# Kernel optimization log

Hardware: AMD Instinct MI355X
Metric: run time of the kernel (lower is better)

Reference implementation:

```python
import jax, jax.numpy as jnp
import numpy as np

NUM_CLASSES = 10
GAMMA = 1.0
EPS = 1e-12


def setup_inputs() -> dict:
    key = jax.random.key(0)
    k1, k2, k3, k4 = jax.random.split(key, 4)
    x = jax.random.normal(k1, (1024, 64), dtype=jnp.float32)
    exemplars = jax.random.normal(k2, (50000, 64), dtype=jnp.float32)
    exemplar_labels = jax.random.randint(k3, (50000,), 0, NUM_CLASSES)
    # beta_raw initialized as softplus^{-1}(init_beta) with init_beta=1.0
    init_beta = 1.0
    beta_raw = jnp.array([np.log(np.exp(init_beta) - 1.0)], dtype=jnp.float32)
    return {"x": x, "exemplars": exemplars, "exemplar_labels": exemplar_labels,
            "beta_raw": beta_raw}


def reference(x, exemplars, exemplar_labels, beta_raw):
    # Squared Euclidean distances (weight_diag == ones) via GEMM expansion:
    # d2[b, e] = ||x_b||^2 + ||e_e||^2 - 2 <x_b, e_e>
    x2 = jnp.sum(x * x, axis=-1, keepdims=True)            # (B, 1)
    e2 = jnp.sum(exemplars * exemplars, axis=-1)           # (Ne,)
    d2 = x2 + e2[None, :] - 2.0 * (x @ exemplars.T)        # (B, Ne)
    d2 = jnp.maximum(d2, 0.0)  # true sq-dist is nonneg; guards GEMM round-off
    beta = jax.nn.softplus(beta_raw[0])
    sims = jnp.exp(-beta * d2)                              # (B, Ne)
    # scatter-add similarities into per-class bins: (C, B) -> (B, C)
    class_sims = jax.ops.segment_sum(sims.T, exemplar_labels,
                                     num_segments=NUM_CLASSES).T
    logits = GAMMA * jnp.log(class_sims + EPS)
    return logits
```

## Files before the change

kernel.cpp:

```cpp
#include <hip/hip_runtime.h>


#define NB      1024
#define NE      50000
#define NE_PAD  50176
#define NCHUNK  98
#define KD      64
#define NC      10
#define SROWS   64
#define NSTAGE  8
#define LROW    72

using half8   = __attribute__((ext_vector_type(8))) _Float16;
using half4v  = __attribute__((ext_vector_type(4))) _Float16;
using floatx4 = __attribute__((ext_vector_type(4))) float;

__device__ __forceinline__ float softplus_f(float x) {
  return (x > 20.f) ? x : log1pf(__expf(x));
}

__global__ __launch_bounds__(256) void prep_kernel(
    const float* __restrict__ x, const float* __restrict__ ex,
    const int* __restrict__ labels, const float* __restrict__ beta_raw,
    _Float16* __restrict__ ex_h, float* __restrict__ ce,
    _Float16* __restrict__ x_h, float* __restrict__ cb,
    int* __restrict__ lab_pad)
{
  const int tid = threadIdx.x;
  const float beta = softplus_f(beta_raw[0]);

  const int row = blockIdx.x * 16 + (tid >> 4);
  const int l16 = tid & 15;

  if (row < NE_PAD) {
    float4 v = make_float4(0.f, 0.f, 0.f, 0.f);
    if (row < NE) v = ((const float4*)ex)[row * 16 + l16];
    half4v hv = { (_Float16)v.x, (_Float16)v.y, (_Float16)v.z, (_Float16)v.w };
    *(half4v*)(ex_h + (size_t)row * KD + l16 * 4) = hv;
    float s = v.x*v.x + v.y*v.y + v.z*v.z + v.w*v.w;
    #pragma unroll
    for (int m = 1; m < 16; m <<= 1) s += __shfl_xor(s, m, 64);
    if (l16 == 0) ce[row] = (row < NE) ? (-beta * s) : -1e30f;
    if (l16 == 1) lab_pad[row] = (row < NE) ? labels[row] : 0;
  } else {
    const int rx = row - NE_PAD;
    float4 v = ((const float4*)x)[rx * 16 + l16];
    half4v hv = { (_Float16)v.x, (_Float16)v.y, (_Float16)v.z, (_Float16)v.w };
    *(half4v*)(x_h + (size_t)rx * KD + l16 * 4) = hv;
    float s = v.x*v.x + v.y*v.y + v.z*v.z + v.w*v.w;
    #pragma unroll
    for (int m = 1; m < 16; m <<= 1) s += __shfl_xor(s, m, 64);
    if (l16 == 0) cb[rx] = -beta * s;
  }
}

__global__ __launch_bounds__(256) void main_kernel(
    const _Float16* __restrict__ ex_h, const float* __restrict__ ce,
    const _Float16* __restrict__ x_h, const float* __restrict__ cb,
    const int* __restrict__ lab_pad, const float* __restrict__ beta_raw,
    float* __restrict__ part)
{
  __shared__ _Float16 Ah[2][SROWS * LROW];
  __shared__ float    Ce[2][SROWS];
  __shared__ int      Lb[2][SROWS];

  const int tid  = threadIdx.x;
  const int wave = tid >> 6;
  const int lane = tid & 63;
  const int l15  = lane & 15;
  const int quad = lane >> 4;

  const int btile = blockIdx.x;
  const int chunk = blockIdx.y;
  const int e0    = chunk * 512;
  const int bm    = btile * 64 + wave * 16;

  const float beta = softplus_f(beta_raw[0]);
  const float s2 = 2.f * beta;

  const half8* xrow = (const half8*)(x_h + (size_t)(bm + l15) * KD);
  const half8 bx0 = xrow[quad];
  const half8 bx1 = xrow[quad + 4];
  const float cbl = cb[bm + l15];

  const int srow = tid >> 2;
  const int scol = tid & 3;
  const _Float16* gsrc = ex_h + (size_t)(e0 + srow) * KD + scol * 16;
  const int lofs = srow * LROW + scol * 16;

  half8 pr0 = *(const half8*)(gsrc);
  half8 pr1 = *(const half8*)(gsrc + 8);
  float prc = 0.f; int prl = 0;
  if (wave == 0) prc = ce[e0 + lane];
  if (wave == 1) prl = lab_pad[e0 + lane];

  *(half8*)(&Ah[0][lofs])     = pr0;
  *(half8*)(&Ah[0][lofs + 8]) = pr1;
  if (wave == 0) Ce[0][lane] = prc;
  if (wave == 1) Lb[0][lane] = prl;
  __syncthreads();

  floatx4 acc = {0.f, 0.f, 0.f, 0.f};

  for (int st = 0; st < NSTAGE; ++st) {
    const int b = st & 1;

    if (st + 1 < NSTAGE) {
      const _Float16* g = gsrc + (size_t)(st + 1) * SROWS * KD;
      pr0 = *(const half8*)(g);
      pr1 = *(const half8*)(g + 8);
      if (wave == 0) prc = ce[e0 + (st + 1) * SROWS + lane];
      if (wave == 1) prl = lab_pad[e0 + (st + 1) * SROWS + lane];
    }

    #pragma unroll
    for (int sub = 0; sub < 4; ++sub) {
      const int abase = (sub * 16 + l15) * LROW + quad * 8;
      const half8 ae0 = *(const half8*)(&Ah[b][abase]);
      const half8 ae1 = *(const half8*)(&Ah[b][abase + 32]);
      const float4 ce4 = *(const float4*)(&Ce[b][sub * 16 + quad * 4]);
      const int4   lb4 = *(const int4*)(&Lb[b][sub * 16 + quad * 4]);

      floatx4 d = {0.f, 0.f, 0.f, 0.f};
      d = __builtin_amdgcn_mfma_f32_16x16x32_f16(ae0, bx0, d, 0, 0, 0);
      d = __builtin_amdgcn_mfma_f32_16x16x32_f16(ae1, bx1, d, 0, 0, 0);

      const float cef[4] = { ce4.x, ce4.y, ce4.z, ce4.w };
      half4v p;
      #pragma unroll
      for (int r = 0; r < 4; ++r) {
        const float t = fminf(fmaf(s2, d[r], cbl + cef[r]), 0.f);
        p[r] = (_Float16)__expf(t);
      }

      half4v oh;
      oh[0] = (lb4.x == l15) ? (_Float16)1.f : (_Float16)0.f;
      oh[1] = (lb4.y == l15) ? (_Float16)1.f : (_Float16)0.f;
      oh[2] = (lb4.z == l15) ? (_Float16)1.f : (_Float16)0.f;
      oh[3] = (lb4.w == l15) ? (_Float16)1.f : (_Float16)0.f;

      acc = __builtin_amdgcn_mfma_f32_16x16x16f16(oh, p, acc, 0, 0, 0);
    }

    if (st + 1 < NSTAGE) {
      __syncthreads();
      const int nb = (st + 1) & 1;
      *(half8*)(&Ah[nb][lofs])     = pr0;
      *(half8*)(&Ah[nb][lofs + 8]) = pr1;
      if (wave == 0) Ce[nb][lane] = prc;
      if (wave == 1) Lb[nb][lane] = prl;
      __syncthreads();
    }
  }

  float* dst = part + (size_t)chunk * (NB * NC);
  #pragma unroll
  for (int r = 0; r < 4; ++r) {
    const int c = quad * 4 + r;
    if (c < NC) {
      dst[(bm + l15) * NC + c] = acc[r];
    }
  }
}

__global__ __launch_bounds__(256) void reduce_kernel(
    const float* __restrict__ part, float* __restrict__ out)
{
  const int bc = blockIdx.x * 256 + threadIdx.x;
  if (bc < NB * NC) {
    float s = 0.f;
    #pragma unroll 7
    for (int k = 0; k < NCHUNK; ++k) s += part[(size_t)k * (NB * NC) + bc];
    out[bc] = __logf(s + 1e-12f);
  }
}

extern "C" void kernel_launch(void* const* d_in, const int* in_sizes, int n_in,
                              void* d_out, int out_size, void* d_ws, size_t ws_size,
                              hipStream_t stream)
{
  const float* x        = (const float*)d_in[0];
  const float* ex       = (const float*)d_in[1];
  const int*   labels   = (const int*)d_in[2];
  const float* beta_raw = (const float*)d_in[3];
  float* out = (float*)d_out;

  char* ws = (char*)d_ws;
  _Float16* ex_h    = (_Float16*)ws;
  float*    ce      = (float*)(ws + 6422528);
  _Float16* x_h     = (_Float16*)(ws + 6623232);
  float*    cb      = (float*)(ws + 6754304);
  int*      lab_pad = (int*)(ws + 6758400);
  float*    part    = (float*)(ws + 6959104);

  prep_kernel<<<3200, 256, 0, stream>>>(x, ex, labels, beta_raw,
                                        ex_h, ce, x_h, cb, lab_pad);
  dim3 g(16, 98);
  main_kernel<<<g, 256, 0, stream>>>(ex_h, ce, x_h, cb, lab_pad, beta_raw, part);
  reduce_kernel<<<40, 256, 0, stream>>>(part, out);
}
```

Before: 102.2 us.

## Process two batch tiles per wave, skip negligible exps, use exp2

Each wave now computes two 16-row batch tiles, so every LDS load of exemplar data feeds twice as many MFMAs, and the grid halves along the batch axis. The beta scaling is pre-multiplied by log2(e) so the hardware exp2 can be used. The exp and the one-hot accumulation MFMAs are skipped whenever every exponent in the wave is below -25 in log2 units, which drops contributions too small to register in fp16. One redundant barrier before the double-buffer write is removed. The costs are higher register pressure and a data-dependent branch whose benefit depends on how far apart the points are.

```diff
diff --git a/kernel.cpp b/kernel.cpp
--- a/kernel.cpp
+++ b/kernel.cpp
@@ -10,6 +10,9 @@
 #define SROWS   64
 #define NSTAGE  8
 #define LROW    72
+#define BCOLS   128
+
+#define LOG2E   1.4426950408889634f
 
 using half8   = __attribute__((ext_vector_type(8))) _Float16;
 using half4v  = __attribute__((ext_vector_type(4))) _Float16;
@@ -17,6 +20,14 @@
 
 __device__ __forceinline__ float softplus_f(float x) {
   return (x > 20.f) ? x : log1pf(__expf(x));
+}
+
+__device__ __forceinline__ float exp2_hw(float x) {
+#if __has_builtin(__builtin_amdgcn_exp2f)
+  return __builtin_amdgcn_exp2f(x);
+#else
+  return exp2f(x);
+#endif
 }
 
 __global__ __launch_bounds__(256) void prep_kernel(
@@ -27,7 +38,7 @@
     int* __restrict__ lab_pad)
 {
   const int tid = threadIdx.x;
-  const float beta = softplus_f(beta_raw[0]);
+  const float nbeta2 = -softplus_f(beta_raw[0]) * LOG2E;
 
   const int row = blockIdx.x * 16 + (tid >> 4);
   const int l16 = tid & 15;
@@ -40,7 +51,7 @@
     float s = v.x*v.x + v.y*v.y + v.z*v.z + v.w*v.w;
     #pragma unroll
     for (int m = 1; m < 16; m <<= 1) s += __shfl_xor(s, m, 64);
-    if (l16 == 0) ce[row] = (row < NE) ? (-beta * s) : -1e30f;
+    if (l16 == 0) ce[row] = (row < NE) ? (nbeta2 * s) : -1e30f;
     if (l16 == 1) lab_pad[row] = (row < NE) ? labels[row] : 0;
   } else {
     const int rx = row - NE_PAD;
@@ -50,7 +61,7 @@
     float s = v.x*v.x + v.y*v.y + v.z*v.z + v.w*v.w;
     #pragma unroll
     for (int m = 1; m < 16; m <<= 1) s += __shfl_xor(s, m, 64);
-    if (l16 == 0) cb[rx] = -beta * s;
+    if (l16 == 0) cb[rx] = nbeta2 * s;
   }
 }
 
@@ -73,15 +84,20 @@
   const int btile = blockIdx.x;
   const int chunk = blockIdx.y;
   const int e0    = chunk * 512;
-  const int bm    = btile * 64 + wave * 16;
+  const int bm0   = btile * BCOLS + wave * 16;
+  const int bm1   = bm0 + 64;
 
   const float beta = softplus_f(beta_raw[0]);
-  const float s2 = 2.f * beta;
-
-  const half8* xrow = (const half8*)(x_h + (size_t)(bm + l15) * KD);
-  const half8 bx0 = xrow[quad];
-  const half8 bx1 = xrow[quad + 4];
-  const float cbl = cb[bm + l15];
+  const float s2 = 2.f * beta * LOG2E;
+
+  const half8* xr0 = (const half8*)(x_h + (size_t)(bm0 + l15) * KD);
+  const half8* xr1 = (const half8*)(x_h + (size_t)(bm1 + l15) * KD);
+  const half8 bx00 = xr0[quad];
+  const half8 bx01 = xr0[quad + 4];
+  const half8 bx10 = xr1[quad];
+  const half8 bx11 = xr1[quad + 4];
+  const float cb0l = cb[bm0 + l15];
+  const float cb1l = cb[bm1 + l15];
 
   const int srow = tid >> 2;
   const int scol = tid & 3;
@@ -100,7 +116,8 @@
   if (wave == 1) Lb[0][lane] = prl;
   __syncthreads();
 
-  floatx4 acc = {0.f, 0.f, 0.f, 0.f};
+  floatx4 acc0 = {0.f, 0.f, 0.f, 0.f};
+  floatx4 acc1 = {0.f, 0.f, 0.f, 0.f};
 
   for (int st = 0; st < NSTAGE; ++st) {
     const int b = st & 1;
@@ -121,29 +138,43 @@
       const float4 ce4 = *(const float4*)(&Ce[b][sub * 16 + quad * 4]);
       const int4   lb4 = *(const int4*)(&Lb[b][sub * 16 + quad * 4]);
 
-      floatx4 d = {0.f, 0.f, 0.f, 0.f};
-      d = __builtin_amdgcn_mfma_f32_16x16x32_f16(ae0, bx0, d, 0, 0, 0);
-      d = __builtin_amdgcn_mfma_f32_16x16x32_f16(ae1, bx1, d, 0, 0, 0);
+      floatx4 d0 = {0.f, 0.f, 0.f, 0.f};
+      floatx4 d1 = {0.f, 0.f, 0.f, 0.f};
+      d0 = __builtin_amdgcn_mfma_f32_16x16x32_f16(ae0, bx00, d0, 0, 0, 0);
+      d0 = __builtin_amdgcn_mfma_f32_16x16x32_f16(ae1, bx01, d0, 0, 0, 0);
+      d1 = __builtin_amdgcn_mfma_f32_16x16x32_f16(ae0, bx10, d1, 0, 0, 0);
+      d1 = __builtin_amdgcn_mfma_f32_16x16x32_f16(ae1, bx11, d1, 0, 0, 0);
 
       const float cef[4] = { ce4.x, ce4.y, ce4.z, ce4.w };
-      half4v p;
+      float t0[4], t1[4];
       #pragma unroll
       for (int r = 0; r < 4; ++r) {
-        const float t = fminf(fmaf(s2, d[r], cbl + cef[r]), 0.f);
-        p[r] = (_Float16)__expf(t);
+        t0[r] = fminf(fmaf(s2, d0[r], cb0l + cef[r]), 0.f);
+        t1[r] = fminf(fmaf(s2, d1[r], cb1l + cef[r]), 0.f);
       }
 
-      half4v oh;
-      oh[0] = (lb4.x == l15) ? (_Float16)1.f : (_Float16)0.f;
-      oh[1] = (lb4.y == l15) ? (_Float16)1.f : (_Float16)0.f;
-      oh[2] = (lb4.z == l15) ? (_Float16)1.f : (_Float16)0.f;
-      oh[3] = (lb4.w == l15) ? (_Float16)1.f : (_Float16)0.f;
-
-      acc = __builtin_amdgcn_mfma_f32_16x16x16f16(oh, p, acc, 0, 0, 0);
+      const float m0 = fmaxf(fmaxf(t0[0], t0[1]), fmaxf(t0[2], t0[3]));
+      const float m1 = fmaxf(fmaxf(t1[0], t1[1]), fmaxf(t1[2], t1[3]));
+      if (__any(fmaxf(m0, m1) > -25.f)) {
+        half4v oh;
+        oh[0] = (lb4.x == l15) ? (_Float16)1.f : (_Float16)0.f;
+        oh[1] = (lb4.y == l15) ? (_Float16)1.f : (_Float16)0.f;
+        oh[2] = (lb4.z == l15) ? (_Float16)1.f : (_Float16)0.f;
+        oh[3] = (lb4.w == l15) ? (_Float16)1.f : (_Float16)0.f;
+
+        half4v p0, p1;
+        #pragma unroll
+        for (int r = 0; r < 4; ++r) {
+          p0[r] = (_Float16)exp2_hw(t0[r]);
+          p1[r] = (_Float16)exp2_hw(t1[r]);
+        }
+
+        acc0 = __builtin_amdgcn_mfma_f32_16x16x16f16(oh, p0, acc0, 0, 0, 0);
+        acc1 = __builtin_amdgcn_mfma_f32_16x16x16f16(oh, p1, acc1, 0, 0, 0);
+      }
     }
 
     if (st + 1 < NSTAGE) {
-      __syncthreads();
       const int nb = (st + 1) & 1;
       *(half8*)(&Ah[nb][lofs])     = pr0;
       *(half8*)(&Ah[nb][lofs + 8]) = pr1;
@@ -158,7 +189,8 @@
   for (int r = 0; r < 4; ++r) {
     const int c = quad * 4 + r;
     if (c < NC) {
-      dst[(bm + l15) * NC + c] = acc[r];
+      dst[(bm0 + l15) * NC + c] = acc0[r];
+      dst[(bm1 + l15) * NC + c] = acc1[r];
     }
   }
 }
@@ -195,7 +227,7 @@
 
   prep_kernel<<<3200, 256, 0, stream>>>(x, ex, labels, beta_raw,
                                         ex_h, ce, x_h, cb, lab_pad);
-  dim3 g(16, 98);
+  dim3 g(NB / BCOLS, NCHUNK);
   main_kernel<<<g, 256, 0, stream>>>(ex_h, ce, x_h, cb, lab_pad, beta_raw, part);
   reduce_kernel<<<40, 256, 0, stream>>>(part, out);
 }
```

After: 94.97 us. 7.1% less time.
